# Kernel tuning notes

Hardware: AMD Instinct MI355X
Metric: run time of the kernel (lower is better)

The kernel has to match this reference:

```python
import jax, jax.numpy as jnp
import numpy as np

B, S, E = 2, 2048, 2048
H, KV, HD = 16, 4, 128          # attn heads, kv heads, head_dim = E//H
GROUPS = H // KV
I = 8192                        # intermediate_size
EPS = 1e-6
ROPE_THETA = 10000.0
SCALE = HD ** -0.5


def _rope_tables(seq_len, head_dim, dtype=jnp.float32):
    inv_freq = 1.0 / (ROPE_THETA ** (jnp.arange(0, head_dim, 2, dtype=jnp.float32) / head_dim))
    pos = jnp.arange(seq_len, dtype=jnp.float32)
    ang = pos[:, None] * inv_freq[None, :]            # [S, HD/2]
    emb = jnp.concatenate([ang, ang], axis=-1)        # [S, HD]
    return jnp.cos(emb).astype(dtype), jnp.sin(emb).astype(dtype)


def _rotate_half(x):
    x1, x2 = jnp.split(x, 2, axis=-1)
    return jnp.concatenate([-x2, x1], axis=-1)


def _apply_rope(x, cos, sin):
    # x: [B, h, S, HD]; cos/sin: [S, HD]
    return x * cos[None, None] + _rotate_half(x) * sin[None, None]


def _rmsnorm(x, w, eps=EPS):
    var = jnp.mean(jnp.square(x), axis=-1, keepdims=True)
    return x * jax.lax.rsqrt(var + eps) * w


def setup_inputs() -> dict:
    key = jax.random.key(0)
    ks = jax.random.split(key, 12)
    sd = lambda fan_in: 1.0 / np.sqrt(fan_in)
    inp = {
        "x": jax.random.normal(ks[0], (B, S, E), dtype=jnp.float32),
        "attn_mask": jnp.zeros((B, 1, S, S), dtype=jnp.bool_),
        "wq": jax.random.normal(ks[1], (E, E), dtype=jnp.float32) * sd(E),
        "bq": jnp.zeros((E,), dtype=jnp.float32),
        "wkv": jax.random.normal(ks[2], (2 * KV * HD, E), dtype=jnp.float32) * sd(E),
        "bkv": jnp.zeros((2 * KV * HD,), dtype=jnp.float32),
        "wo": jax.random.normal(ks[3], (E, E), dtype=jnp.float32) * sd(E),
        "w_gate": jax.random.normal(ks[4], (I, E), dtype=jnp.float32) * sd(E),
        "w_up": jax.random.normal(ks[5], (I, E), dtype=jnp.float32) * sd(E),
        "w_down": jax.random.normal(ks[6], (E, I), dtype=jnp.float32) * sd(I),
        "norm1_w": jnp.ones((E,), dtype=jnp.float32),
        "norm2_w": jnp.ones((E,), dtype=jnp.float32),
    }
    return inp


def reference(x, attn_mask, wq, bq, wkv, bkv, wo, w_gate, w_up, w_down, norm1_w, norm2_w):
    # ---- attention block ----
    y = _rmsnorm(x, norm1_w)
    q = y @ wq.T + bq                                     # [B,S,E]
    kv = y @ wkv.T + bkv                                  # [B,S,2*KV*HD]
    k, v = jnp.split(kv, 2, axis=-1)
    q = q.reshape(B, S, H, HD).transpose(0, 2, 1, 3)      # [B,H,S,HD]
    k = k.reshape(B, S, KV, HD).transpose(0, 2, 1, 3)     # [B,KV,S,HD]
    v = v.reshape(B, S, KV, HD).transpose(0, 2, 1, 3)
    cos, sin = _rope_tables(S, HD, dtype=q.dtype)
    q = _apply_rope(q, cos, sin)
    k = _apply_rope(k, cos, sin)
    # GQA expand kv heads
    k = jnp.repeat(k, GROUPS, axis=1)                     # [B,H,S,HD]
    v = jnp.repeat(v, GROUPS, axis=1)
    # NOTE: source Qwen2Attention.forward never applies attn_mask — faithful here.
    scores = jnp.einsum('bhsd,bhtd->bhst', q, k) * SCALE  # [B,H,S,S]
    attn = jax.nn.softmax(scores, axis=-1)
    o = jnp.einsum('bhst,bhtd->bhsd', attn, v)            # [B,H,S,HD]
    o = o.transpose(0, 2, 1, 3).reshape(B, S, E) @ wo.T
    x = x + o
    # ---- MLP block (SwiGLU) ----
    y = _rmsnorm(x, norm2_w)
    h = jax.nn.silu(y @ w_gate.T) * (y @ w_up.T)          # [B,S,I]
    x = x + h @ w_down.T
    return x
```

## Files before the change

### kernel.cpp

```cpp
#include <hip/hip_runtime.h>

typedef __bf16 bf16;
typedef __bf16 bf16x8 __attribute__((ext_vector_type(8)));
typedef __bf16 bf16x4 __attribute__((ext_vector_type(4)));
typedef float f32x4 __attribute__((ext_vector_type(4)));

#define DEV __device__ __forceinline__

constexpr int B_ = 2, S_ = 2048, E_ = 2048, H_ = 16, KVH_ = 4, HD_ = 128, I_ = 8192;
constexpr int KVROW = 2 * KVH_ * HD_;
constexpr float EPS_ = 1e-6f;
constexpr float SCALE_ = 0.08838834764831845f;

DEV void gload_lds16(const bf16* g, bf16* l) {
  __builtin_amdgcn_global_load_lds(
      (const __attribute__((address_space(1))) void*)g,
      (__attribute__((address_space(3))) void*)l, 16, 0, 0);
}

__global__ __launch_bounds__(256) void cvt6_k(const float* __restrict__ s0, const float* __restrict__ s1,
                                              const float* __restrict__ s2, const float* __restrict__ s3,
                                              const float* __restrict__ s4, const float* __restrict__ s5,
                                              bf16* __restrict__ dst) {
  constexpr size_t N0 = 4194304, N1 = 2097152, N2 = 4194304,
                   N3 = 16777216, N4 = 16777216, N5 = 16777216;
  constexpr size_t TOT = N0 + N1 + N2 + N3 + N4 + N5;
  for (size_t i = ((size_t)blockIdx.x * 256 + threadIdx.x) * 8; i < TOT;
       i += (size_t)gridDim.x * 256 * 8) {
    size_t off = i; const float* sp;
    if (off < N0) sp = s0;
    else if ((off -= N0) < N1) sp = s1;
    else if ((off -= N1) < N2) sp = s2;
    else if ((off -= N2) < N3) sp = s3;
    else if ((off -= N3) < N4) sp = s4;
    else { off -= N4; sp = s5; }
    const float4* p = (const float4*)(sp + off);
    float4 a = p[0], b = p[1];
    bf16x8 o;
    o[0]=(bf16)a.x; o[1]=(bf16)a.y; o[2]=(bf16)a.z; o[3]=(bf16)a.w;
    o[4]=(bf16)b.x; o[5]=(bf16)b.y; o[6]=(bf16)b.z; o[7]=(bf16)b.w;
    *(bf16x8*)(dst + i) = o;
  }
}

template <typename InT>
__global__ __launch_bounds__(256) void rmsnorm_k(const InT* __restrict__ x,
                                                 const float* __restrict__ w,
                                                 bf16* __restrict__ y) {
  const int row = blockIdx.x, t = threadIdx.x;
  const size_t base = (size_t)row * E_ + t * 8;
  float v[8];
  if constexpr (sizeof(InT) == 2) {
    bf16x8 d = *(const bf16x8*)(x + base);
#pragma unroll
    for (int j = 0; j < 8; ++j) v[j] = (float)d[j];
  } else {
    const float4* p = (const float4*)(x + base);
    float4 a = p[0], b2 = p[1];
    v[0]=a.x; v[1]=a.y; v[2]=a.z; v[3]=a.w; v[4]=b2.x; v[5]=b2.y; v[6]=b2.z; v[7]=b2.w;
  }
  float ss = 0.f;
#pragma unroll
  for (int j = 0; j < 8; ++j) ss += v[j] * v[j];
#pragma unroll
  for (int off = 32; off; off >>= 1) ss += __shfl_xor(ss, off);
  __shared__ float red[4];
  if ((t & 63) == 0) red[t >> 6] = ss;
  __syncthreads();
  ss = red[0] + red[1] + red[2] + red[3];
  const float sc = rsqrtf(ss * (1.0f / E_) + EPS_);
  const float4* wp = (const float4*)(w + t * 8);
  float4 wa = wp[0], wb = wp[1];
  float wv[8] = {wa.x, wa.y, wa.z, wa.w, wb.x, wb.y, wb.z, wb.w};
  bf16x8 o;
#pragma unroll
  for (int j = 0; j < 8; ++j) o[j] = (bf16)(v[j] * sc * wv[j]);
  *(bf16x8*)(y + base) = o;
}

__global__ __launch_bounds__(256) void rope_k(bf16* __restrict__ q, bf16* __restrict__ kvb) {
  const int gid = blockIdx.x * 256 + threadIdx.x;
  const int d = gid & 63;
  const int r = gid >> 6;
  const int hh = r % (H_ + KVH_);
  const int s = (r / (H_ + KVH_)) % S_;
  const int b = r / ((H_ + KVH_) * S_);
  bf16* p = (hh < H_) ? (q + (size_t)(b * S_ + s) * E_ + hh * HD_)
                      : (kvb + (size_t)(b * S_ + s) * KVROW + (hh - H_) * HD_);
  const float invf = exp2f(-(float)d * (13.287712379549449f / 64.f));
  float sn, cs;
  sincosf((float)s * invf, &sn, &cs);
  const float x1 = (float)p[d], x2 = (float)p[d + 64];
  p[d] = (bf16)(x1 * cs - x2 * sn);
  p[d + 64] = (bf16)(x2 * cs + x1 * sn);
}

__global__ __launch_bounds__(256, 2) void gemm_gu(const bf16* __restrict__ A,
                                                  const bf16* __restrict__ Wg,
                                                  const bf16* __restrict__ Wu,
                                                  bf16* __restrict__ out,
                                                  int M, int N, int K) {
  constexpr int BK = 64;
  __shared__ bf16 As[128 * BK];
  __shared__ bf16 Bg[128 * BK];
  __shared__ bf16 Bu[128 * BK];
  const int t = threadIdx.x, lane = t & 63, w = t >> 6;
  const int g = lane >> 4, l15 = lane & 15;
  const int bm = blockIdx.y, bn = blockIdx.x;
  const int wm = w >> 1, wn = w & 1;
  f32x4 ag[4][4], au[4][4];
#pragma unroll
  for (int i = 0; i < 4; ++i)
#pragma unroll
    for (int j = 0; j < 4; ++j) { ag[i][j] = {0.f,0.f,0.f,0.f}; au[i][j] = {0.f,0.f,0.f,0.f}; }

  const bf16* Ab  = A  + (size_t)bm * 128 * K;
  const bf16* Wgb = Wg + (size_t)bn * 128 * K;
  const bf16* Wub = Wu + (size_t)bn * 128 * K;

  for (int k0 = 0; k0 < K; k0 += BK) {
    __syncthreads();
#pragma unroll
    for (int i = 0; i < 4; ++i) {
      const int c = t + i * 256;
      const int row = c >> 3, slot = c & 7;
      const size_t goff = (size_t)row * K + k0 + ((slot ^ (row & 7)) << 3);
      gload_lds16(Ab + goff, &As[c * 8]);
      gload_lds16(Wgb + goff, &Bg[c * 8]);
      gload_lds16(Wub + goff, &Bu[c * 8]);
    }
    __syncthreads();
#pragma unroll
    for (int ks = 0; ks < 2; ++ks) {
      bf16x8 af[4], bgv[4], buv[4];
#pragma unroll
      for (int mt = 0; mt < 4; ++mt) {
        const int row = wm * 64 + mt * 16 + l15;
        af[mt] = *(const bf16x8*)&As[row * BK + (((ks * 4 + g) ^ (row & 7)) << 3)];
      }
#pragma unroll
      for (int nt = 0; nt < 4; ++nt) {
        const int row = wn * 64 + nt * 16 + l15;
        const int off = row * BK + (((ks * 4 + g) ^ (row & 7)) << 3);
        bgv[nt] = *(const bf16x8*)&Bg[off];
        buv[nt] = *(const bf16x8*)&Bu[off];
      }
#pragma unroll
      for (int mt = 0; mt < 4; ++mt)
#pragma unroll
        for (int nt = 0; nt < 4; ++nt) {
          ag[mt][nt] = __builtin_amdgcn_mfma_f32_16x16x32_bf16(af[mt], bgv[nt], ag[mt][nt], 0, 0, 0);
          au[mt][nt] = __builtin_amdgcn_mfma_f32_16x16x32_bf16(af[mt], buv[nt], au[mt][nt], 0, 0, 0);
        }
    }
  }

  const int row0 = bm * 128 + wm * 64;
  const int col0 = bn * 128 + wn * 64;
#pragma unroll
  for (int nt = 0; nt < 4; ++nt) {
    const int col = col0 + nt * 16 + l15;
#pragma unroll
    for (int mt = 0; mt < 4; ++mt) {
#pragma unroll
      for (int r = 0; r < 4; ++r) {
        const int rowi = row0 + mt * 16 + g * 4 + r;
        const float gv = ag[mt][nt][r];
        const float hv = (gv / (1.f + __expf(-gv))) * au[mt][nt][r];
        out[(size_t)rowi * N + col] = (bf16)hv;
      }
    }
  }
}

template <int EPI, bool WB>
__global__ __launch_bounds__(256, 2) void gemm_bt(const bf16* __restrict__ A,
                                                  const void* __restrict__ Wp,
                                                  const float* __restrict__ bias,
                                                  const void* __restrict__ ext,
                                                  void* __restrict__ out,
                                                  int M, int N, int K) {
  constexpr int BK = 64;
  __shared__ bf16 As[128 * BK];
  __shared__ bf16 Bs[128 * BK];
  const int t = threadIdx.x, lane = t & 63, w = t >> 6;
  const int g = lane >> 4, l15 = lane & 15;
  const int bm = blockIdx.y, bn = blockIdx.x;
  const int wm = w >> 1, wn = w & 1;
  f32x4 acc[4][4];
#pragma unroll
  for (int i = 0; i < 4; ++i)
#pragma unroll
    for (int j = 0; j < 4; ++j) acc[i][j] = {0.f, 0.f, 0.f, 0.f};

  const bf16* Ab = A + (size_t)bm * 128 * K;

  for (int k0 = 0; k0 < K; k0 += BK) {
    __syncthreads();
#pragma unroll
    for (int i = 0; i < 4; ++i) {
      const int c = t + i * 256;
      const int row = c >> 3, slot = c & 7;
      gload_lds16(Ab + (size_t)row * K + k0 + ((slot ^ (row & 7)) << 3), &As[c * 8]);
    }
    if constexpr (WB) {
      const bf16* Wb = (const bf16*)Wp + (size_t)bn * 128 * K;
#pragma unroll
      for (int i = 0; i < 4; ++i) {
        const int c = t + i * 256;
        const int row = c >> 3, slot = c & 7;
        gload_lds16(Wb + (size_t)row * K + k0 + ((slot ^ (row & 7)) << 3), &Bs[c * 8]);
      }
    } else {
      const float* Wb = (const float*)Wp + (size_t)bn * 128 * K;
#pragma unroll
      for (int i = 0; i < 4; ++i) {
        const int c = t + i * 256;
        const int row = c >> 3, slot = c & 7;
        const float4* wp = (const float4*)(Wb + (size_t)row * K + k0 + slot * 8);
        float4 w0 = wp[0], w1 = wp[1];
        bf16x8 pk;
        pk[0] = (bf16)w0.x; pk[1] = (bf16)w0.y; pk[2] = (bf16)w0.z; pk[3] = (bf16)w0.w;
        pk[4] = (bf16)w1.x; pk[5] = (bf16)w1.y; pk[6] = (bf16)w1.z; pk[7] = (bf16)w1.w;
        *(bf16x8*)&Bs[row * BK + ((slot ^ (row & 7)) << 3)] = pk;
      }
    }
    __syncthreads();
#pragma unroll
    for (int ks = 0; ks < 2; ++ks) {
      bf16x8 af[4], bfv[4];
#pragma unroll
      for (int mt = 0; mt < 4; ++mt) {
        const int row = wm * 64 + mt * 16 + l15;
        af[mt] = *(const bf16x8*)&As[row * BK + (((ks * 4 + g) ^ (row & 7)) << 3)];
      }
#pragma unroll
      for (int nt = 0; nt < 4; ++nt) {
        const int row = wn * 64 + nt * 16 + l15;
        bfv[nt] = *(const bf16x8*)&Bs[row * BK + (((ks * 4 + g) ^ (row & 7)) << 3)];
      }
#pragma unroll
      for (int mt = 0; mt < 4; ++mt)
#pragma unroll
        for (int nt = 0; nt < 4; ++nt)
          acc[mt][nt] = __builtin_amdgcn_mfma_f32_16x16x32_bf16(af[mt], bfv[nt], acc[mt][nt], 0, 0, 0);
    }
  }

  const int row0 = bm * 128 + wm * 64;
  const int col0 = bn * 128 + wn * 64;
#pragma unroll
  for (int nt = 0; nt < 4; ++nt) {
    const int col = col0 + nt * 16 + l15;
    const float bv = bias ? bias[col] : 0.f;
#pragma unroll
    for (int mt = 0; mt < 4; ++mt) {
#pragma unroll
      for (int r = 0; r < 4; ++r) {
        const int rowi = row0 + mt * 16 + g * 4 + r;
        const size_t idx = (size_t)rowi * N + col;
        float v = acc[mt][nt][r] + bv;
        if constexpr (EPI == 0) {
          ((bf16*)out)[idx] = (bf16)v;
        } else if constexpr (EPI == 1) {
          v += ((const float*)ext)[idx];
          ((bf16*)out)[idx] = (bf16)v;
        } else if constexpr (EPI == 2) {
          const float gv = (float)((const bf16*)ext)[idx];
          const float sg = gv / (1.f + __expf(-gv));
          ((bf16*)out)[idx] = (bf16)(sg * v);
        } else {
          v += (float)((const bf16*)ext)[idx];
          ((float*)out)[idx] = v;
        }
      }
    }
  }
}

__global__ __launch_bounds__(256, 2) void attn_k(const bf16* __restrict__ qb,
                                                 const bf16* __restrict__ kvb,
                                                 bf16* __restrict__ ob) {
  __shared__ bf16 Ks[64 * 128];
  __shared__ bf16 Vt[128 * 64];
  __shared__ bf16 Ps[4][32 * 64];
  const int t = threadIdx.x, lane = t & 63, w = t >> 6;
  const int g = lane >> 4, l15 = lane & 15;
  const int b = blockIdx.z, h = blockIdx.y;
  const int kvh = h >> 2;
  const int q0 = blockIdx.x * 128 + w * 32;

  bf16x8 qf[2][4];
#pragma unroll
  for (int qt = 0; qt < 2; ++qt)
#pragma unroll
    for (int ks = 0; ks < 4; ++ks)
      qf[qt][ks] = *(const bf16x8*)(qb + (size_t)(b * S_ + q0 + qt * 16 + l15) * E_ + h * HD_ + ks * 32 + g * 8);

  f32x4 o[8][2];
#pragma unroll
  for (int i = 0; i < 8; ++i) { o[i][0] = {0.f,0.f,0.f,0.f}; o[i][1] = {0.f,0.f,0.f,0.f}; }
  float mA[2] = {-1e30f, -1e30f}, lA[2] = {0.f, 0.f};

  for (int s0 = 0; s0 < S_; s0 += 64) {
    __syncthreads();
#pragma unroll
    for (int i = 0; i < 4; ++i) {
      const int c = t + i * 256;
      const int row = c >> 4, slot = c & 15;
      gload_lds16(kvb + (size_t)(b * S_ + s0 + row) * KVROW + kvh * HD_ + ((slot ^ (row & 15)) << 3),
                  &Ks[c * 8]);
    }
#pragma unroll
    for (int i = 0; i < 4; ++i) {
      const int c = t + i * 256;
      const int d = c & 127, kvc = c >> 7;
      const bf16* vs = kvb + (size_t)(b * S_ + s0 + kvc * 8) * KVROW + KVH_ * HD_ + kvh * HD_ + d;
      bf16x8 pk;
#pragma unroll
      for (int j = 0; j < 8; ++j) pk[j] = vs[(size_t)j * KVROW];
      *(bf16x8*)&Vt[d * 64 + ((kvc ^ (d & 7)) << 3)] = pk;
    }
    __syncthreads();

    f32x4 sc[2][4];
#pragma unroll
    for (int qt = 0; qt < 2; ++qt)
#pragma unroll
      for (int c = 0; c < 4; ++c) sc[qt][c] = {0.f,0.f,0.f,0.f};
#pragma unroll
    for (int ks = 0; ks < 4; ++ks) {
      bf16x8 kf[4];
#pragma unroll
      for (int c = 0; c < 4; ++c) {
        const int kv = c * 16 + l15;
        kf[c] = *(const bf16x8*)&Ks[kv * 128 + (((ks * 4 + g) ^ (kv & 15)) << 3)];
      }
#pragma unroll
      for (int c = 0; c < 4; ++c) {
        sc[0][c] = __builtin_amdgcn_mfma_f32_16x16x32_bf16(kf[c], qf[0][ks], sc[0][c], 0, 0, 0);
        sc[1][c] = __builtin_amdgcn_mfma_f32_16x16x32_bf16(kf[c], qf[1][ks], sc[1][c], 0, 0, 0);
      }
    }

    float corr[2];
#pragma unroll
    for (int qt = 0; qt < 2; ++qt) {
      float tm = sc[qt][0][0];
#pragma unroll
      for (int c = 0; c < 4; ++c)
#pragma unroll
        for (int r = 0; r < 4; ++r) tm = fmaxf(tm, sc[qt][c][r]);
      tm = fmaxf(tm, __shfl_xor(tm, 16));
      tm = fmaxf(tm, __shfl_xor(tm, 32));
      const float mn = fmaxf(mA[qt], tm);
      corr[qt] = __expf((mA[qt] - mn) * SCALE_);
      mA[qt] = mn;
      float ps = 0.f;
      const int q = qt * 16 + l15;
#pragma unroll
      for (int c = 0; c < 4; ++c)
#pragma unroll
        for (int r = 0; r < 4; ++r) {
          const float p = __expf((sc[qt][c][r] - mn) * SCALE_);
          ps += p;
          const int kv = c * 16 + g * 4 + r;
          Ps[w][q * 64 + (((kv >> 3) ^ (q & 7)) << 3) + (kv & 7)] = (bf16)p;
        }
      ps += __shfl_xor(ps, 16);
      ps += __shfl_xor(ps, 32);
      lA[qt] = lA[qt] * corr[qt] + ps;
#pragma unroll
      for (int dt = 0; dt < 8; ++dt) o[dt][qt] *= corr[qt];
    }
    asm volatile("s_waitcnt lgkmcnt(0)" ::: "memory");
#pragma unroll
    for (int ks = 0; ks < 2; ++ks) {
      bf16x8 pf[2];
#pragma unroll
      for (int qt = 0; qt < 2; ++qt) {
        const int q = qt * 16 + l15;
        pf[qt] = *(const bf16x8*)&Ps[w][q * 64 + (((ks * 4 + g) ^ (q & 7)) << 3)];
      }
#pragma unroll
      for (int dt = 0; dt < 8; ++dt) {
        const int d = dt * 16 + l15;
        const bf16x8 vf = *(const bf16x8*)&Vt[d * 64 + (((ks * 4 + g) ^ (d & 7)) << 3)];
        o[dt][0] = __builtin_amdgcn_mfma_f32_16x16x32_bf16(vf, pf[0], o[dt][0], 0, 0, 0);
        o[dt][1] = __builtin_amdgcn_mfma_f32_16x16x32_bf16(vf, pf[1], o[dt][1], 0, 0, 0);
      }
    }
  }

  const float inv0 = 1.f / lA[0], inv1 = 1.f / lA[1];
  __syncthreads();
  bf16* bb = (w < 2) ? &Ks[(w & 1) * 4096] : &Vt[(w & 1) * 4096];
#pragma unroll
  for (int dt = 0; dt < 8; ++dt)
#pragma unroll
    for (int qt = 0; qt < 2; ++qt) {
      const float iv = qt ? inv1 : inv0;
      bf16x4 pk;
#pragma unroll
      for (int r = 0; r < 4; ++r) pk[r] = (bf16)(o[dt][qt][r] * iv);
      const int q = qt * 16 + l15;
      const int s16 = (dt * 2 + (g >> 1)) ^ (q & 15);
      *(bf16x4*)&bb[q * 128 + (s16 << 3) + ((g & 1) << 2)] = pk;
    }
  asm volatile("s_waitcnt lgkmcnt(0)" ::: "memory");
#pragma unroll
  for (int it = 0; it < 8; ++it) {
    const int c = lane + it * 64;
    const int q = c >> 4, s16 = c & 15;
    const bf16x8 vv = *(const bf16x8*)&bb[q * 128 + ((s16 ^ (q & 15)) << 3)];
    *(bf16x8*)(ob + (size_t)(b * S_ + q0 + q) * E_ + h * HD_ + s16 * 8) = vv;
  }
}

extern "C" void kernel_launch(void* const* d_in, const int* in_sizes, int n_in,
                              void* d_out, int out_size, void* d_ws, size_t ws_size,
                              hipStream_t stream) {
  const float* x   = (const float*)d_in[0];
  const float* wq  = (const float*)d_in[2];
  const float* bq  = (const float*)d_in[3];
  const float* wkv = (const float*)d_in[4];
  const float* bkv = (const float*)d_in[5];
  const float* wo  = (const float*)d_in[6];
  const float* wg  = (const float*)d_in[7];
  const float* wu  = (const float*)d_in[8];
  const float* wd  = (const float*)d_in[9];
  const float* n1  = (const float*)d_in[10];
  const float* n2  = (const float*)d_in[11];
  float* out = (float*)d_out;
  char* ws = (char*)d_ws;
  bf16* y  = (bf16*)(ws);
  bf16* q  = (bf16*)(ws + (16ull << 20));
  bf16* kv = (bf16*)(ws + (32ull << 20));
  bf16* x1 = (bf16*)(ws + (40ull << 20));
  bf16* gh = (bf16*)(ws + (56ull << 20));
  bf16* o  = y;
  bf16* y2 = y;
  bf16* wqb  = (bf16*)(ws + (120ull << 20));
  bf16* wkvb = (bf16*)(ws + (128ull << 20));
  bf16* wob  = (bf16*)(ws + (132ull << 20));
  bf16* wgb  = (bf16*)(ws + (140ull << 20));
  bf16* wub  = (bf16*)(ws + (172ull << 20));
  bf16* wdb  = (bf16*)(ws + (204ull << 20));
  const int M = B_ * S_;
  const bool tierA = ws_size >= (236ull << 20);

  if (tierA)
    cvt6_k<<<2048, 256, 0, stream>>>(wq, wkv, wo, wg, wu, wd, wqb);

  rmsnorm_k<float><<<M, 256, 0, stream>>>(x, n1, y);
  if (tierA) {
    gemm_bt<0, true><<<dim3(E_ / 128, M / 128), 256, 0, stream>>>(y, wqb, bq, nullptr, q, M, E_, E_);
    gemm_bt<0, true><<<dim3(KVROW / 128, M / 128), 256, 0, stream>>>(y, wkvb, bkv, nullptr, kv, M, KVROW, E_);
  } else {
    gemm_bt<0, false><<<dim3(E_ / 128, M / 128), 256, 0, stream>>>(y, wq, bq, nullptr, q, M, E_, E_);
    gemm_bt<0, false><<<dim3(KVROW / 128, M / 128), 256, 0, stream>>>(y, wkv, bkv, nullptr, kv, M, KVROW, E_);
  }
  rope_k<<<(B_ * S_ * (H_ + KVH_) * 64) / 256, 256, 0, stream>>>(q, kv);
  attn_k<<<dim3(S_ / 128, H_, B_), 256, 0, stream>>>(q, kv, o);
  if (tierA) {
    gemm_bt<1, true><<<dim3(E_ / 128, M / 128), 256, 0, stream>>>(o, wob, nullptr, x, x1, M, E_, E_);
    rmsnorm_k<bf16><<<M, 256, 0, stream>>>(x1, n2, y2);
    gemm_gu<<<dim3(I_ / 128, M / 128), 256, 0, stream>>>(y2, wgb, wub, gh, M, I_, E_);
    gemm_bt<3, true><<<dim3(E_ / 128, M / 128), 256, 0, stream>>>(gh, wdb, nullptr, x1, out, M, E_, I_);
  } else {
    gemm_bt<1, false><<<dim3(E_ / 128, M / 128), 256, 0, stream>>>(o, wo, nullptr, x, x1, M, E_, E_);
    rmsnorm_k<bf16><<<M, 256, 0, stream>>>(x1, n2, y2);
    gemm_bt<0, false><<<dim3(I_ / 128, M / 128), 256, 0, stream>>>(y2, wg, nullptr, nullptr, gh, M, I_, E_);
    gemm_bt<2, false><<<dim3(I_ / 128, M / 128), 256, 0, stream>>>(y2, wu, nullptr, gh, gh, M, I_, E_);
    gemm_bt<3, false><<<dim3(E_ / 128, M / 128), 256, 0, stream>>>(gh, wd, nullptr, x1, out, M, E_, I_);
  }
}
```

Measured before the change: 754.9 us.

## Use 256x128 tiles with 8 waves for o-proj, gate/up and down GEMMs

```diff
diff --git a/kernel.cpp b/kernel.cpp
--- a/kernel.cpp
+++ b/kernel.cpp
@@ -95,13 +95,13 @@
   p[d + 64] = (bf16)(x2 * cs + x1 * sn);
 }
 
-__global__ __launch_bounds__(256, 2) void gemm_gu(const bf16* __restrict__ A,
-                                                  const bf16* __restrict__ Wg,
-                                                  const bf16* __restrict__ Wu,
-                                                  bf16* __restrict__ out,
-                                                  int M, int N, int K) {
+__global__ __launch_bounds__(512, 2) void gemm_guw(const bf16* __restrict__ A,
+                                                   const bf16* __restrict__ Wg,
+                                                   const bf16* __restrict__ Wu,
+                                                   bf16* __restrict__ out,
+                                                   int M, int N, int K) {
   constexpr int BK = 64;
-  __shared__ bf16 As[128 * BK];
+  __shared__ bf16 As[256 * BK];
   __shared__ bf16 Bg[128 * BK];
   __shared__ bf16 Bu[128 * BK];
   const int t = threadIdx.x, lane = t & 63, w = t >> 6;
@@ -114,7 +114,7 @@
 #pragma unroll
     for (int j = 0; j < 4; ++j) { ag[i][j] = {0.f,0.f,0.f,0.f}; au[i][j] = {0.f,0.f,0.f,0.f}; }
 
-  const bf16* Ab  = A  + (size_t)bm * 128 * K;
+  const bf16* Ab  = A  + (size_t)bm * 256 * K;
   const bf16* Wgb = Wg + (size_t)bn * 128 * K;
   const bf16* Wub = Wu + (size_t)bn * 128 * K;
 
@@ -122,10 +122,15 @@
     __syncthreads();
 #pragma unroll
     for (int i = 0; i < 4; ++i) {
-      const int c = t + i * 256;
+      const int c = t + i * 512;
+      const int row = c >> 3, slot = c & 7;
+      gload_lds16(Ab + (size_t)row * K + k0 + ((slot ^ (row & 7)) << 3), &As[c * 8]);
+    }
+#pragma unroll
+    for (int i = 0; i < 2; ++i) {
+      const int c = t + i * 512;
       const int row = c >> 3, slot = c & 7;
       const size_t goff = (size_t)row * K + k0 + ((slot ^ (row & 7)) << 3);
-      gload_lds16(Ab + goff, &As[c * 8]);
       gload_lds16(Wgb + goff, &Bg[c * 8]);
       gload_lds16(Wub + goff, &Bu[c * 8]);
     }
@@ -155,7 +160,7 @@
     }
   }
 
-  const int row0 = bm * 128 + wm * 64;
+  const int row0 = bm * 256 + wm * 64;
   const int col0 = bn * 128 + wn * 64;
 #pragma unroll
   for (int nt = 0; nt < 4; ++nt) {
@@ -168,6 +173,88 @@
         const float gv = ag[mt][nt][r];
         const float hv = (gv / (1.f + __expf(-gv))) * au[mt][nt][r];
         out[(size_t)rowi * N + col] = (bf16)hv;
+      }
+    }
+  }
+}
+
+template <int EPI>
+__global__ __launch_bounds__(512, 2) void gemm_w(const bf16* __restrict__ A,
+                                                 const bf16* __restrict__ W,
+                                                 const void* __restrict__ ext,
+                                                 void* __restrict__ out,
+                                                 int M, int N, int K) {
+  constexpr int BK = 64;
+  __shared__ bf16 As[256 * BK];
+  __shared__ bf16 Bs[128 * BK];
+  const int t = threadIdx.x, lane = t & 63, w = t >> 6;
+  const int g = lane >> 4, l15 = lane & 15;
+  const int bm = blockIdx.y, bn = blockIdx.x;
+  const int wm = w >> 1, wn = w & 1;
+  f32x4 acc[4][4];
+#pragma unroll
+  for (int i = 0; i < 4; ++i)
+#pragma unroll
+    for (int j = 0; j < 4; ++j) acc[i][j] = {0.f, 0.f, 0.f, 0.f};
+
+  const bf16* Ab = A + (size_t)bm * 256 * K;
+  const bf16* Wb = W + (size_t)bn * 128 * K;
+
+  for (int k0 = 0; k0 < K; k0 += BK) {
+    __syncthreads();
+#pragma unroll
+    for (int i = 0; i < 4; ++i) {
+      const int c = t + i * 512;
+      const int row = c >> 3, slot = c & 7;
+      gload_lds16(Ab + (size_t)row * K + k0 + ((slot ^ (row & 7)) << 3), &As[c * 8]);
+    }
+#pragma unroll
+    for (int i = 0; i < 2; ++i) {
+      const int c = t + i * 512;
+      const int row = c >> 3, slot = c & 7;
+      gload_lds16(Wb + (size_t)row * K + k0 + ((slot ^ (row & 7)) << 3), &Bs[c * 8]);
+    }
+    __syncthreads();
+#pragma unroll
+    for (int ks = 0; ks < 2; ++ks) {
+      bf16x8 af[4], bfv[4];
+#pragma unroll
+      for (int mt = 0; mt < 4; ++mt) {
+        const int row = wm * 64 + mt * 16 + l15;
+        af[mt] = *(const bf16x8*)&As[row * BK + (((ks * 4 + g) ^ (row & 7)) << 3)];
+      }
+#pragma unroll
+      for (int nt = 0; nt < 4; ++nt) {
+        const int row = wn * 64 + nt * 16 + l15;
+        bfv[nt] = *(const bf16x8*)&Bs[row * BK + (((ks * 4 + g) ^ (row & 7)) << 3)];
+      }
+#pragma unroll
+      for (int mt = 0; mt < 4; ++mt)
+#pragma unroll
+        for (int nt = 0; nt < 4; ++nt)
+          acc[mt][nt] = __builtin_amdgcn_mfma_f32_16x16x32_bf16(af[mt], bfv[nt], acc[mt][nt], 0, 0, 0);
+    }
+  }
+
+  const int row0 = bm * 256 + wm * 64;
+  const int col0 = bn * 128 + wn * 64;
+#pragma unroll
+  for (int nt = 0; nt < 4; ++nt) {
+    const int col = col0 + nt * 16 + l15;
+#pragma unroll
+    for (int mt = 0; mt < 4; ++mt) {
+#pragma unroll
+      for (int r = 0; r < 4; ++r) {
+        const int rowi = row0 + mt * 16 + g * 4 + r;
+        const size_t idx = (size_t)rowi * N + col;
+        float v = acc[mt][nt][r];
+        if constexpr (EPI == 1) {
+          v += ((const float*)ext)[idx];
+          ((bf16*)out)[idx] = (bf16)v;
+        } else {
+          v += (float)((const bf16*)ext)[idx];
+          ((float*)out)[idx] = v;
+        }
       }
     }
   }
@@ -463,10 +550,10 @@
   rope_k<<<(B_ * S_ * (H_ + KVH_) * 64) / 256, 256, 0, stream>>>(q, kv);
   attn_k<<<dim3(S_ / 128, H_, B_), 256, 0, stream>>>(q, kv, o);
   if (tierA) {
-    gemm_bt<1, true><<<dim3(E_ / 128, M / 128), 256, 0, stream>>>(o, wob, nullptr, x, x1, M, E_, E_);
+    gemm_w<1><<<dim3(E_ / 128, M / 256), 512, 0, stream>>>(o, wob, x, x1, M, E_, E_);
     rmsnorm_k<bf16><<<M, 256, 0, stream>>>(x1, n2, y2);
-    gemm_gu<<<dim3(I_ / 128, M / 128), 256, 0, stream>>>(y2, wgb, wub, gh, M, I_, E_);
-    gemm_bt<3, true><<<dim3(E_ / 128, M / 128), 256, 0, stream>>>(gh, wdb, nullptr, x1, out, M, E_, I_);
+    gemm_guw<<<dim3(I_ / 128, M / 256), 512, 0, stream>>>(y2, wgb, wub, gh, M, I_, E_);
+    gemm_w<3><<<dim3(E_ / 128, M / 256), 512, 0, stream>>>(gh, wdb, x1, out, M, E_, I_);
   } else {
     gemm_bt<1, false><<<dim3(E_ / 128, M / 128), 256, 0, stream>>>(o, wo, nullptr, x, x1, M, E_, E_);
     rmsnorm_k<bf16><<<M, 256, 0, stream>>>(x1, n2, y2);
```

Result: slower. 893.0 us (+18.3%).
